# Kernel tuning notes

Measured on AMD Instinct MI355X. Metric: run time of the kernel, lower is better.

## Reference

```python
import jax, jax.numpy as jnp
import numpy as np

B, T, C = 4, 2048, 1024
N_HEADS = 16
HEAD_DIM = C // N_HEADS


def setup_inputs() -> dict:
    key = jax.random.key(0)
    k1, k2, k3, k4, k5 = jax.random.split(key, 5)
    x = jax.random.normal(k1, (B, T, C), dtype=jnp.float32)
    # torch Linear: y = x @ W.T + b; store W as [out, in]
    w_qkv = jax.random.normal(k2, (3 * C, C), dtype=jnp.float32) * (1.0 / np.sqrt(C))
    b_qkv = jax.random.normal(k3, (3 * C,), dtype=jnp.float32) * 0.01
    w_proj = jax.random.normal(k4, (C, C), dtype=jnp.float32) * (1.0 / np.sqrt(C))
    b_proj = jax.random.normal(k5, (C,), dtype=jnp.float32) * 0.01
    return {"x": x, "w_qkv": w_qkv, "b_qkv": b_qkv, "w_proj": w_proj, "b_proj": b_proj}


def reference(x, w_qkv, b_qkv, w_proj, b_proj):
    Bx, Tx, Cx = x.shape
    scale = 1.0 / np.sqrt(HEAD_DIM)
    qkv = x @ w_qkv.T + b_qkv                              # [B,T,3C]
    qkv = qkv.reshape(Bx, Tx, 3, N_HEADS, HEAD_DIM)
    qkv = jnp.transpose(qkv, (2, 0, 3, 1, 4))              # [3,B,H,T,D]
    q, k, v = qkv[0], qkv[1], qkv[2]
    att = jnp.einsum('bhqd,bhkd->bhqk', q, k) * scale      # [B,H,T,T]
    causal = jnp.tril(jnp.ones((Tx, Tx), dtype=bool))
    att = jnp.where(causal[None, None, :, :], att, -jnp.inf)
    att = jax.nn.softmax(att, axis=-1)
    # dropout p=0.0 (eval) -> identity
    out = jnp.einsum('bhqk,bhkd->bhqd', att, v)            # [B,H,T,D]
    out = jnp.transpose(out, (0, 2, 1, 3)).reshape(Bx, Tx, Cx)
    return out @ w_proj.T + b_proj
```

## Files before the change

kernel.cpp:

```cpp
#include <hip/hip_runtime.h>
#include <hip/hip_bf16.h>
#include <cstdint>

typedef __attribute__((ext_vector_type(8))) short bf16x8;
typedef __attribute__((ext_vector_type(4))) float f32x4;
typedef __attribute__((ext_vector_type(16))) float f32x16;

#define MFMA16(a, b, c) __builtin_amdgcn_mfma_f32_16x16x32_bf16(a, b, c, 0, 0, 0)
#define MFMA32(a, b, c) __builtin_amdgcn_mfma_f32_32x32x16_bf16(a, b, c, 0, 0, 0)

typedef __attribute__((address_space(1))) uint32_t as1_u32;
typedef __attribute__((address_space(3))) uint32_t as3_u32;
static __device__ __forceinline__ void gload16(const void* g, void* l) {
  __builtin_amdgcn_global_load_lds((as1_u32*)g, (as3_u32*)l, 16, 0, 0);
}

static __device__ __forceinline__ ushort f2b(float f) {
  union { float f; uint32_t u; } v; v.f = f;
  uint32_t u = v.u;
  uint32_t r = (u + 0x7FFFu + ((u >> 16) & 1u)) >> 16;
  return (ushort)r;
}

static __device__ __forceinline__ uint32_t cvtpk(float a, float b) {
  uint32_t r;
  asm("v_cvt_pk_bf16_f32 %0, %1, %2" : "=v"(r) : "v"(a), "v"(b));
  return r;
}
static __device__ __forceinline__ void plswap(uint32_t& a, uint32_t& b) {
  asm volatile("v_permlane32_swap_b32 %0, %1" : "+v"(a), "+v"(b));
}

#define QSCALE 0.1803368782f

#define LOFF(r, kc4) (((r) >> 1) * 64 + ((((((r) & 1) << 2) | (kc4)) ^ (((r) >> 1) & 7)) * 8))

#define N4_X  2097152
#define N4_WQ 786432
#define N4_WP 262144
__global__ void cvt_all(const float* __restrict__ x, const float* __restrict__ wq,
                        const float* __restrict__ wp, ushort* __restrict__ xb,
                        ushort* __restrict__ wqb, ushort* __restrict__ wpb) {
  int i = blockIdx.x * blockDim.x + threadIdx.x;
  const float* src; ushort* dst; int j;
  if (i < N4_X)            { src = x;  dst = xb;  j = i; }
  else if (i < N4_X + N4_WQ) { src = wq; dst = wqb; j = i - N4_X; }
  else                     { src = wp; dst = wpb; j = i - (N4_X + N4_WQ); }
  const float4 v = ((const float4*)src)[j];
  ushort4 o;
  o.x = f2b(v.x); o.y = f2b(v.y); o.z = f2b(v.z); o.w = f2b(v.w);
  ((ushort4*)dst)[j] = o;
}

__global__ __launch_bounds__(512, 2) void gemm_qkv256(
    const ushort* __restrict__ A,
    const ushort* __restrict__ W,
    const float* __restrict__ bias,
    int M, int N, int K,
    ushort* __restrict__ q_ws, ushort* __restrict__ k_ws, ushort* __restrict__ v_ws) {
  __shared__ ushort As[2][2][2][64 * 64];
  __shared__ ushort Bs[2][2][2][64 * 64];
  const int tid = threadIdx.x;
  const int cpx = gridDim.x >> 3;
  const int wg = (blockIdx.x & 7) * cpx + (blockIdx.x >> 3);
  const int m0 = (wg / 12) * 256, n0 = (wg % 12) * 256;
  const int wid = tid >> 6, lane = tid & 63;
  const int wr = wid >> 2, wc = wid & 3;
  const int lr = lane & 15, lg = lane >> 4;
  const int bhalf = wc >> 1, brow = (wc & 1) * 64;
  const int prow = tid >> 3, pchk = tid & 7;
  const int lchk = pchk ^ (prow & 7);
  const int srow = prow * 2 + (lchk >> 2);
  const int skc = (lchk & 3) * 8;

  f32x4 acc[8][4] = {};
  const int nt = K >> 6;

#define STA(db_, half_, kt_)                                                  \
  { const ushort* src = A + (size_t)(m0 + (half_)*128 + srow) * K + (kt_)*64 + skc; \
    gload16(src, &As[db_][half_][0][tid * 8]);                                \
    gload16(src + 32, &As[db_][half_][1][tid * 8]); }
#define STB(db_, half_, kt_)                                                  \
  { const ushort* src = W + (size_t)(n0 + (half_)*128 + srow) * K + (kt_)*64 + skc; \
    gload16(src, &Bs[db_][half_][0][tid * 8]);                                \
    gload16(src + 32, &Bs[db_][half_][1][tid * 8]); }

  STB(0, 0, 0); STB(0, 1, 0);
  STA(0, 0, 0); STA(0, 1, 0);
  STB(1, 0, 1); STB(1, 1, 1);
  asm volatile("s_waitcnt vmcnt(4)" ::: "memory");
  __builtin_amdgcn_s_barrier();

  for (int T = 0; T < nt; ++T) {
    const int db = T & 1;
    const ushort* Ak0 = &As[db][wr][0][0];
    const ushort* Ak1 = &As[db][wr][1][0];
    const ushort* Bk0 = &Bs[db][bhalf][0][0];
    const ushort* Bk1 = &Bs[db][bhalf][1][0];
    bf16x8 b[4][2];
    {
      bf16x8 a[4][2];
#pragma unroll
      for (int mm = 0; mm < 4; ++mm) {
        const int r = mm * 16 + lr;
        a[mm][0] = *(const bf16x8*)&Ak0[LOFF(r, lg)];
        a[mm][1] = *(const bf16x8*)&Ak1[LOFF(r, lg)];
      }
#pragma unroll
      for (int nf = 0; nf < 4; ++nf) {
        const int rr = brow + nf * 16 + lr;
        b[nf][0] = *(const bf16x8*)&Bk0[LOFF(rr, lg)];
        b[nf][1] = *(const bf16x8*)&Bk1[LOFF(rr, lg)];
      }
      if (T + 1 < nt) { STA(db ^ 1, 0, T + 1); STA(db ^ 1, 1, T + 1); }
      __builtin_amdgcn_sched_barrier(0);
      __builtin_amdgcn_s_barrier();
      asm volatile("s_waitcnt lgkmcnt(0)" ::: "memory");
      __builtin_amdgcn_sched_barrier(0);
      __builtin_amdgcn_s_setprio(1);
#pragma unroll
      for (int kk = 0; kk < 2; ++kk)
#pragma unroll
        for (int mm = 0; mm < 4; ++mm)
#pragma unroll
          for (int nf = 0; nf < 4; ++nf)
            acc[mm][nf] = MFMA16(a[mm][kk], b[nf][kk], acc[mm][nf]);
      __builtin_amdgcn_s_setprio(0);
      __builtin_amdgcn_s_barrier();
    }
    {
      bf16x8 a[4][2];
#pragma unroll
      for (int mm = 0; mm < 4; ++mm) {
        const int r = (4 + mm) * 16 + lr;
        a[mm][0] = *(const bf16x8*)&Ak0[LOFF(r, lg)];
        a[mm][1] = *(const bf16x8*)&Ak1[LOFF(r, lg)];
      }
      if (T + 2 < nt) { STB(db, 0, T + 2); STB(db, 1, T + 2); }
      __builtin_amdgcn_sched_barrier(0);
      __builtin_amdgcn_s_barrier();
      asm volatile("s_waitcnt lgkmcnt(0)" ::: "memory");
      __builtin_amdgcn_sched_barrier(0);
      __builtin_amdgcn_s_setprio(1);
#pragma unroll
      for (int kk = 0; kk < 2; ++kk)
#pragma unroll
        for (int mm = 0; mm < 4; ++mm)
#pragma unroll
          for (int nf = 0; nf < 4; ++nf)
            acc[4 + mm][nf] = MFMA16(a[mm][kk], b[nf][kk], acc[4 + mm][nf]);
      __builtin_amdgcn_s_setprio(0);
      if (T + 2 < nt)
        asm volatile("s_waitcnt vmcnt(4)" ::: "memory");
      else if (T + 1 < nt)
        asm volatile("s_waitcnt vmcnt(0)" ::: "memory");
      if (T + 1 < nt) __builtin_amdgcn_s_barrier();
    }
  }
#undef STA
#undef STB

#pragma unroll
  for (int mf = 0; mf < 8; ++mf) {
#pragma unroll
    for (int nf = 0; nf < 4; ++nf) {
      const int rowb = m0 + wr * 128 + mf * 16 + lg * 4;
      const int col = n0 + wc * 64 + nf * 16 + lr;
      float v[4];
#pragma unroll
      for (int i = 0; i < 4; ++i) v[i] = acc[mf][nf][i] + bias[col];
      const int sel = col >> 10;
      const int rem = col & 1023;
      const int h = rem >> 6, d = rem & 63;
      const int bb = rowb >> 11, t0 = rowb & 2047;
      if (sel == 2) {
        ushort4 st;
        st.x = f2b(v[0]); st.y = f2b(v[1]); st.z = f2b(v[2]); st.w = f2b(v[3]);
        *(ushort4*)&v_ws[((size_t)(bb * 16 + h) * 64 + d) * 2048 + t0] = st;
      } else if (sel == 0) {
#pragma unroll
        for (int i = 0; i < 4; ++i)
          q_ws[((size_t)(bb * 16 + h) * 2048 + t0 + i) * 64 + d] = f2b(v[i] * QSCALE);
      } else {
#pragma unroll
        for (int i = 0; i < 4; ++i)
          k_ws[((size_t)(bb * 16 + h) * 2048 + t0 + i) * 64 + d] = f2b(v[i]);
      }
    }
  }
}

__global__ __launch_bounds__(512, 2) void gemm_proj(
    const ushort* __restrict__ A,
    const ushort* __restrict__ W,
    const float* __restrict__ bias,
    int M, int N, int K,
    float* __restrict__ out) {
  __shared__ ushort As[2][2][64 * 64];
  __shared__ ushort Bs[2][2][2][64 * 64];
  const int tid = threadIdx.x;
  const int nbx = N >> 8;
  const int cpx = gridDim.x >> 3;
  const int wg = (blockIdx.x & 7) * cpx + (blockIdx.x >> 3);
  const int m0 = (wg / nbx) * 128, n0 = (wg % nbx) * 256;
  const int wid = tid >> 6, lane = tid & 63;
  const int wr = wid >> 2, wc = wid & 3;
  const int lr = lane & 15, lg = lane >> 4;
  const int prow = tid >> 3, pchk = tid & 7;
  const int lchk = pchk ^ (prow & 7);
  const int srow = prow * 2 + (lchk >> 2);
  const int skc = (lchk & 3) * 8;

  f32x4 acc[4][4] = {};
  const int nt = K >> 6;

#define STA(db_, kt_)                                                         \
  { const ushort* src = A + (size_t)(m0 + srow) * K + (kt_)*64 + skc;         \
    gload16(src, &As[db_][0][tid * 8]);                                       \
    gload16(src + 32, &As[db_][1][tid * 8]); }
#define STB(db_, half_, kt_)                                                  \
  { const ushort* src = W + (size_t)(n0 + (half_)*128 + srow) * K + (kt_)*64 + skc; \
    gload16(src, &Bs[db_][half_][0][tid * 8]);                                \
    gload16(src + 32, &Bs[db_][half_][1][tid * 8]); }

  STB(0, 0, 0); STB(0, 1, 0);
  STA(0, 0);
  STB(1, 0, 1); STB(1, 1, 1);
  asm volatile("s_waitcnt vmcnt(4)" ::: "memory");
  __builtin_amdgcn_s_barrier();

  const int bhalf = wc >> 1, brow = (wc & 1) * 64;
  for (int T = 0; T < nt; ++T) {
    const int db = T & 1;
    const ushort* Asub0 = &As[db][0][0];
    const ushort* Asub1 = &As[db][1][0];
    const ushort* Bsub0 = &Bs[db][bhalf][0][0];
    const ushort* Bsub1 = &Bs[db][bhalf][1][0];
    bf16x8 b[4][2];
    {
      bf16x8 a[2][2];
#pragma unroll
      for (int mm = 0; mm < 2; ++mm) {
        const int r = wr * 64 + mm * 16 + lr;
        a[mm][0] = *(const bf16x8*)&Asub0[LOFF(r, lg)];
        a[mm][1] = *(const bf16x8*)&Asub1[LOFF(r, lg)];
      }
#pragma unroll
      for (int nf = 0; nf < 4; ++nf) {
        const int r = brow + nf * 16 + lr;
        b[nf][0] = *(const bf16x8*)&Bsub0[LOFF(r, lg)];
        b[nf][1] = *(const bf16x8*)&Bsub1[LOFF(r, lg)];
      }
      if (T + 1 < nt) STA((T + 1) & 1, T + 1);
      __builtin_amdgcn_sched_barrier(0);
      __builtin_amdgcn_s_barrier();
      asm volatile("s_waitcnt lgkmcnt(0)" ::: "memory");
      __builtin_amdgcn_sched_barrier(0);
      __builtin_amdgcn_s_setprio(1);
#pragma unroll
      for (int kk = 0; kk < 2; ++kk)
#pragma unroll
        for (int mm = 0; mm < 2; ++mm)
#pragma unroll
          for (int nf = 0; nf < 4; ++nf)
            acc[mm][nf] = MFMA16(a[mm][kk], b[nf][kk], acc[mm][nf]);
      __builtin_amdgcn_s_setprio(0);
      __builtin_amdgcn_s_barrier();
    }
    {
      bf16x8 a[2][2];
#pragma unroll
      for (int mm = 0; mm < 2; ++mm) {
        const int r = wr * 64 + (2 + mm) * 16 + lr;
        a[mm][0] = *(const bf16x8*)&Asub0[LOFF(r, lg)];
        a[mm][1] = *(const bf16x8*)&Asub1[LOFF(r, lg)];
      }
      if (T + 2 < nt) { STB(db, 0, T + 2); STB(db, 1, T + 2); }
      __builtin_amdgcn_sched_barrier(0);
      __builtin_amdgcn_s_barrier();
      asm volatile("s_waitcnt lgkmcnt(0)" ::: "memory");
      __builtin_amdgcn_sched_barrier(0);
      __builtin_amdgcn_s_setprio(1);
#pragma unroll
      for (int kk = 0; kk < 2; ++kk)
#pragma unroll
        for (int mm = 0; mm < 2; ++mm)
#pragma unroll
          for (int nf = 0; nf < 4; ++nf)
            acc[2 + mm][nf] = MFMA16(a[mm][kk], b[nf][kk], acc[2 + mm][nf]);
      __builtin_amdgcn_s_setprio(0);
      if (T + 2 < nt)
        asm volatile("s_waitcnt vmcnt(4)" ::: "memory");
      else if (T + 1 < nt)
        asm volatile("s_waitcnt vmcnt(0)" ::: "memory");
      if (T + 1 < nt) __builtin_amdgcn_s_barrier();
    }
  }
#undef STA
#undef STB

#pragma unroll
  for (int mf = 0; mf < 4; ++mf) {
#pragma unroll
    for (int nf = 0; nf < 4; ++nf) {
      const int rowb = m0 + wr * 64 + mf * 16 + lg * 4;
      const int col = n0 + wc * 64 + nf * 16 + lr;
#pragma unroll
      for (int i = 0; i < 4; ++i)
        out[(size_t)(rowb + i) * N + col] = acc[mf][nf][i] + bias[col];
    }
  }
}

__global__ __launch_bounds__(256, 4) void attn_v6(
    const ushort* __restrict__ Q, const ushort* __restrict__ K,
    const ushort* __restrict__ VT, ushort* __restrict__ O ) {
  const int blk = blockIdx.x;
  const int s = 15 - (blk >> 6);
  const int bh = blk & 63;
  const int tid = threadIdx.x;
  const int w = tid >> 6, lane = tid & 63;
  const int l31 = lane & 31, l5 = lane >> 5;
  const int bb = bh >> 4, h = bh & 15;
  const size_t base = (size_t)bh * 2048 * 64;
  const ushort* Qb = Q + base;
  const ushort* Kb = K + base;
  const ushort* VTb = VT + base;

  __shared__ ushort Ks[2][64 * 64];
  __shared__ ushort Vs[2][64 * 64];
  __shared__ float l_lds[4][32];

#define STAGE(buf, kt_)                                              \
  do {                                                               \
    const ushort* Kt = Kb + (size_t)(kt_) * 64 * 64;                 \
    const ushort* Vt = VTb + (kt_) * 64;                             \
    _Pragma("unroll") for (int i_ = 0; i_ < 2; ++i_) {               \
      const int ch = i_ * 256 + tid;                                 \
      const int r = ch >> 3;                                         \
      const int csw = ((ch & 7) ^ (r & 7)) * 8;                      \
      gload16(&Kt[(size_t)r * 64 + csw], &Ks[buf][ch * 8]);          \
      gload16(&Vt[(size_t)r * 2048 + csw], &Vs[buf][ch * 8]);        \
    }                                                                \
  } while (0)

  const int q0w = s * 128 + w * 32;
  const int nt = 2 * s + 2;
  const int qlane = q0w + l31;

  bf16x8 qf[4];
#pragma unroll
  for (int dblk = 0; dblk < 4; ++dblk)
    qf[dblk] = *(const bf16x8*)&Qb[(size_t)qlane * 64 + dblk * 16 + l5 * 8];

  f32x16 o0 = {}, o1 = {};
  float lsum = 0.f;

  STAGE(0, 0);
  __syncthreads();

  for (int kt = 0; kt < nt; ++kt) {
    const int cur = kt & 1;
    if (kt + 1 < nt) STAGE(cur ^ 1, kt + 1);
    const int k0 = kt << 6;
    const ushort* Ksc = Ks[cur];
    const ushort* Vsc = Vs[cur];
#pragma unroll
    for (int kblk = 0; kblk < 2; ++kblk) {
      const int kbase = k0 + kblk * 32;
      if (kbase <= q0w + 31) {
        f32x16 st = {};
        __builtin_amdgcn_s_setprio(1);
#pragma unroll
        for (int dblk = 0; dblk < 4; ++dblk) {
          const int row = kblk * 32 + l31;
          bf16x8 ka = *(const bf16x8*)&Ksc[row * 64 + (((dblk * 2 + l5) ^ (row & 7)) * 8)];
          st = MFMA32(ka, qf[dblk], st);
        }
        __builtin_amdgcn_s_setprio(0);
        if (kbase + 31 > q0w) {
#pragma unroll
          for (int r = 0; r < 16; ++r) {
            const int kk = kbase + (r & 3) + 8 * (r >> 2) + 4 * l5;
            st[r] = (kk <= qlane) ? st[r] : -INFINITY;
          }
        }
        float p[16];
#pragma unroll
        for (int r = 0; r < 16; ++r) {
          p[r] = __builtin_amdgcn_exp2f(st[r]);
          lsum += p[r];
        }
#pragma unroll
        for (int sbl = 0; sbl < 2; ++sbl) {
          uint32_t P0 = cvtpk(p[8 * sbl + 0], p[8 * sbl + 1]);
          uint32_t P1 = cvtpk(p[8 * sbl + 2], p[8 * sbl + 3]);
          uint32_t P2 = cvtpk(p[8 * sbl + 4], p[8 * sbl + 5]);
          uint32_t P3 = cvtpk(p[8 * sbl + 6], p[8 * sbl + 7]);
          plswap(P0, P2);
          plswap(P1, P3);
          union { uint32_t u[4]; bf16x8 v; } pk;
          pk.u[0] = P0; pk.u[1] = P1; pk.u[2] = P2; pk.u[3] = P3;
          const int kchunk = kblk * 4 + sbl * 2 + l5;
          __builtin_amdgcn_s_setprio(1);
#pragma unroll
          for (int db2 = 0; db2 < 2; ++db2) {
            const int vrow = db2 * 32 + l31;
            bf16x8 vb = *(const bf16x8*)&Vsc[vrow * 64 + ((kchunk ^ (vrow & 7)) * 8)];
            if (db2 == 0) o0 = MFMA32(pk.v, vb, o0);
            else          o1 = MFMA32(pk.v, vb, o1);
          }
          __builtin_amdgcn_s_setprio(0);
        }
      }
    }
    __syncthreads();
  }

  const float lfull = lsum + __shfl_xor(lsum, 32);
  if (lane < 32) l_lds[w][lane] = 1.f / lfull;
#pragma unroll
  for (int r = 0; r < 16; ++r) {
    const int qoff = (r & 3) + 8 * (r >> 2) + 4 * l5;
    const float inv = l_lds[w][qoff];
    const int t = q0w + qoff;
    ushort* op = &O[(size_t)(bb * 2048 + t) * 1024 + h * 64 + l31];
    op[0] = f2b(o0[r] * inv);
    op[32] = f2b(o1[r] * inv);
  }
#undef STAGE
}

extern "C" void kernel_launch(void* const* d_in, const int* in_sizes, int n_in,
                              void* d_out, int out_size, void* d_ws, size_t ws_size,
                              hipStream_t stream) {
  const float* x = (const float*)d_in[0];
  const float* w_qkv = (const float*)d_in[1];
  const float* b_qkv = (const float*)d_in[2];
  const float* w_proj = (const float*)d_in[3];
  const float* b_proj = (const float*)d_in[4];
  float* out = (float*)d_out;

  char* ws = (char*)d_ws;
  const size_t SZ_X = (size_t)8192 * 1024 * 2;
  const size_t SZ_WQ = (size_t)3072 * 1024 * 2;
  const size_t SZ_WP = (size_t)1024 * 1024 * 2;
  ushort* xb = (ushort*)(ws);
  ushort* wqb = (ushort*)(ws + SZ_X);
  ushort* wpb = (ushort*)(ws + SZ_X + SZ_WQ);
  ushort* q_ws = (ushort*)(ws + SZ_X + SZ_WQ + SZ_WP);
  ushort* k_ws = q_ws + (size_t)8192 * 1024;
  ushort* v_ws = k_ws + (size_t)8192 * 1024;

  cvt_all<<<(N4_X + N4_WQ + N4_WP) / 256, 256, 0, stream>>>(
      x, w_qkv, w_proj, xb, wqb, wpb);

  gemm_qkv256<<<384, 512, 0, stream>>>(
      xb, wqb, b_qkv, 8192, 3072, 1024, q_ws, k_ws, v_ws);

  attn_v6<<<1024, 256, 0, stream>>>(q_ws, k_ws, v_ws, xb);

  gemm_proj<<<256, 512, 0, stream>>>(
      xb, wpb, b_proj, 8192, 1024, 1024, out);
}
```

Baseline: 157.4 us.

## Split QKV GEMM into full-wave 256-tile and 128-tile launches to fix wave quantization

The QKV projection previously ran 384 256x256 tiles, which do not map evenly onto the CU count. It now runs 256 large tiles for the first 2048 output columns, then a second launch of 256 smaller 128x256 tiles for the V columns. The second launch reuses a templated version of the projection GEMM with the QKV scatter epilogue. This aims to remove the partial-wave tail, at the cost of an extra launch and lower per-tile reuse in the second phase.

```diff
diff --git a/kernel.cpp b/kernel.cpp
--- a/kernel.cpp
+++ b/kernel.cpp
@@ -56,14 +56,14 @@
     const ushort* __restrict__ A,
     const ushort* __restrict__ W,
     const float* __restrict__ bias,
-    int M, int N, int K,
+    int K, int nbx, int nbase,
     ushort* __restrict__ q_ws, ushort* __restrict__ k_ws, ushort* __restrict__ v_ws) {
   __shared__ ushort As[2][2][2][64 * 64];
   __shared__ ushort Bs[2][2][2][64 * 64];
   const int tid = threadIdx.x;
   const int cpx = gridDim.x >> 3;
   const int wg = (blockIdx.x & 7) * cpx + (blockIdx.x >> 3);
-  const int m0 = (wg / 12) * 256, n0 = (wg % 12) * 256;
+  const int m0 = (wg / nbx) * 256, n0 = nbase + (wg % nbx) * 256;
   const int wid = tid >> 6, lane = tid & 63;
   const int wr = wid >> 2, wc = wid & 3;
   const int lr = lane & 15, lg = lane >> 4;
@@ -190,19 +190,20 @@
   }
 }
 
-__global__ __launch_bounds__(512, 2) void gemm_proj(
+template<int EPI>
+__global__ __launch_bounds__(512, 2) void gemm_2ph(
     const ushort* __restrict__ A,
     const ushort* __restrict__ W,
     const float* __restrict__ bias,
-    int M, int N, int K,
+    int K, int Nout, int nbx, int nbase,
+    ushort* __restrict__ q_ws, ushort* __restrict__ k_ws, ushort* __restrict__ v_ws,
     float* __restrict__ out) {
   __shared__ ushort As[2][2][64 * 64];
   __shared__ ushort Bs[2][2][2][64 * 64];
   const int tid = threadIdx.x;
-  const int nbx = N >> 8;
   const int cpx = gridDim.x >> 3;
   const int wg = (blockIdx.x & 7) * cpx + (blockIdx.x >> 3);
-  const int m0 = (wg / nbx) * 128, n0 = (wg % nbx) * 256;
+  const int m0 = (wg / nbx) * 128, n0 = nbase + (wg % nbx) * 256;
   const int wid = tid >> 6, lane = tid & 63;
   const int wr = wid >> 2, wc = wid & 3;
   const int lr = lane & 15, lg = lane >> 4;
@@ -305,9 +306,32 @@
     for (int nf = 0; nf < 4; ++nf) {
       const int rowb = m0 + wr * 64 + mf * 16 + lg * 4;
       const int col = n0 + wc * 64 + nf * 16 + lr;
-#pragma unroll
-      for (int i = 0; i < 4; ++i)
-        out[(size_t)(rowb + i) * N + col] = acc[mf][nf][i] + bias[col];
+      float v[4];
+#pragma unroll
+      for (int i = 0; i < 4; ++i) v[i] = acc[mf][nf][i] + bias[col];
+      if (EPI == 0) {
+        const int sel = col >> 10;
+        const int rem = col & 1023;
+        const int h = rem >> 6, d = rem & 63;
+        const int bb = rowb >> 11, t0 = rowb & 2047;
+        if (sel == 2) {
+          ushort4 st;
+          st.x = f2b(v[0]); st.y = f2b(v[1]); st.z = f2b(v[2]); st.w = f2b(v[3]);
+          *(ushort4*)&v_ws[((size_t)(bb * 16 + h) * 64 + d) * 2048 + t0] = st;
+        } else if (sel == 0) {
+#pragma unroll
+          for (int i = 0; i < 4; ++i)
+            q_ws[((size_t)(bb * 16 + h) * 2048 + t0 + i) * 64 + d] = f2b(v[i] * QSCALE);
+        } else {
+#pragma unroll
+          for (int i = 0; i < 4; ++i)
+            k_ws[((size_t)(bb * 16 + h) * 2048 + t0 + i) * 64 + d] = f2b(v[i]);
+        }
+      } else {
+#pragma unroll
+        for (int i = 0; i < 4; ++i)
+          out[(size_t)(rowb + i) * Nout + col] = v[i];
+      }
     }
   }
 }
@@ -455,11 +479,14 @@
   cvt_all<<<(N4_X + N4_WQ + N4_WP) / 256, 256, 0, stream>>>(
       x, w_qkv, w_proj, xb, wqb, wpb);
 
-  gemm_qkv256<<<384, 512, 0, stream>>>(
-      xb, wqb, b_qkv, 8192, 3072, 1024, q_ws, k_ws, v_ws);
+  gemm_qkv256<<<256, 512, 0, stream>>>(
+      xb, wqb, b_qkv, 1024, 8, 0, q_ws, k_ws, v_ws);
+
+  gemm_2ph<0><<<256, 512, 0, stream>>>(
+      xb, wqb, b_qkv, 1024, 0, 4, 2048, q_ws, k_ws, v_ws, nullptr);
 
   attn_v6<<<1024, 256, 0, stream>>>(q_ws, k_ws, v_ws, xb);
 
-  gemm_proj<<<256, 512, 0, stream>>>(
-      xb, wpb, b_proj, 8192, 1024, 1024, out);
-}
+  gemm_2ph<1><<<256, 512, 0, stream>>>(
+      xb, wpb, b_proj, 1024, 1024, 4, 0, nullptr, nullptr, nullptr, out);
+}
```

After: 153.0 us. 1.03x faster.
